# Optimization experiments

Hardware: AMD Instinct MI355X
Metric: run time of the kernel (lower is better)

Reference implementation:

```python
import jax, jax.numpy as jnp
import numpy as np

N = 2500   # total_neurons
K = 50     # connections_per_neuron
T = 60     # temporal_sequence
F = 5      # input_features
H = 128    # lstm hidden_size
B = 512    # batch
GROUPS = [800, 700, 600, 400]  # support_resistance, trend_detection, pattern_recognition, volume_analysis


def _lstm_layer(x, Wih, Whh, bih, bhh):
    # x: [B, T, D]; PyTorch gate order (i, f, g, o); eval mode (no dropout)
    bs = x.shape[0]
    h0 = jnp.zeros((bs, H), x.dtype)

    def step(carry, xt):
        h, c = carry
        g = xt @ Wih.T + h @ Whh.T + bih + bhh
        i, f, gg, o = jnp.split(g, 4, axis=-1)
        c = jax.nn.sigmoid(f) * c + jax.nn.sigmoid(i) * jnp.tanh(gg)
        h = jax.nn.sigmoid(o) * jnp.tanh(c)
        return (h, c), h

    (h, c), ys = jax.lax.scan(step, (h0, h0), jnp.swapaxes(x, 0, 1))
    return jnp.swapaxes(ys, 0, 1), h


def _forward(x, W_ih0, W_hh0, b_ih0, b_hh0, W_ih1, W_hh1, b_ih1, b_hh1,
             fp_w1, fp_b1, fp_w2, fp_b2, conn_w, sens, thr,
             int_w1, int_b1, int_w2, int_b2, int_w3, int_b3,
             tw, tb, pw, pb, kw, kb, vw, vb, cw, cb, conn_idx):
    y0, _ = _lstm_layer(x, W_ih0, W_hh0, b_ih0, b_hh0)
    _, hlast = _lstm_layer(y0, W_ih1, W_hh1, b_ih1, b_hh1)        # hidden[-1]: [B, H]
    base = jnp.tanh(jax.nn.relu(hlast @ fp_w1.T + fp_b1) @ fp_w2.T + fp_b2)  # [B, 32]
    # all_activations = base repeated over N neurons; each neuron reduces its
    # K gathered activations (weighted) and the identical 32 feature dims to a scalar.
    feat_sum = base.sum(-1)                                        # [B]
    acts = jnp.broadcast_to(feat_sum[:, None], (x.shape[0], N))    # [B, N]
    gathered = acts[:, conn_idx]                                   # [B, N, K] irregular gather
    wi = jnp.einsum('bnk,nk->bn', gathered, conn_w)                # [B, N]
    pre = wi * sens
    o0 = GROUPS[0]; o1 = o0 + GROUPS[1]; o2 = o1 + GROUPS[2]
    neuron_out = jnp.concatenate([
        jax.nn.sigmoid(pre[:, :o0] - thr[:o0]),                    # support_resistance
        jnp.tanh(pre[:, o0:o1]),                                   # trend_detection
        jax.nn.relu(pre[:, o1:o2] - thr[o1:o2]),                   # pattern_recognition
        jax.nn.sigmoid(pre[:, o2:]),                               # volume_analysis
    ], axis=1)                                                     # [B, N]
    h1 = jax.nn.relu(neuron_out @ int_w1.T + int_b1)
    h2 = jax.nn.relu(h1 @ int_w2.T + int_b2)
    integrated = jnp.tanh(h2 @ int_w3.T + int_b3)                  # [B, 32]
    trend = integrated @ tw.T + tb                                 # [B, 3]
    patt = integrated @ pw.T + pb                                  # [B, 6]
    keyl = integrated @ kw.T + kb                                  # [B, 4]
    vol = integrated @ vw.T + vb                                   # [B, 1]
    conf = integrated @ cw.T + cb                                  # [B, 1]
    means = jnp.stack([neuron_out[:, :o0].mean(1), neuron_out[:, o0:o1].mean(1),
                       neuron_out[:, o1:o2].mean(1), neuron_out[:, o2:].mean(1)], axis=-1)
    # heads(15) + raw confidence(1) + overall_confidence(1) + specialty means(4) -> [B, 21]? no: 3+6+4+1+1+1+4 = 20
    return jnp.concatenate([trend, patt, keyl, vol, conf, jax.nn.sigmoid(conf), means], axis=-1)


def setup_inputs() -> dict:
    key = jax.random.key(0)
    ks = jax.random.split(key, 40)
    rn = lambda k, s, sc=0.1: jax.random.normal(k, s, dtype=jnp.float32) * sc
    inp = {}
    inp['x'] = jax.random.normal(ks[0], (B, T, F), dtype=jnp.float32)
    inp['W_ih0'] = rn(ks[1], (4 * H, F)); inp['W_hh0'] = rn(ks[2], (4 * H, H))
    inp['b_ih0'] = rn(ks[3], (4 * H,));   inp['b_hh0'] = rn(ks[4], (4 * H,))
    inp['W_ih1'] = rn(ks[5], (4 * H, H)); inp['W_hh1'] = rn(ks[6], (4 * H, H))
    inp['b_ih1'] = rn(ks[7], (4 * H,));   inp['b_hh1'] = rn(ks[8], (4 * H,))
    inp['fp_w1'] = rn(ks[9], (64, H));    inp['fp_b1'] = rn(ks[10], (64,))
    inp['fp_w2'] = rn(ks[11], (32, 64));  inp['fp_b2'] = rn(ks[12], (32,))
    inp['conn_w'] = rn(ks[13], (N, K))
    inp['sens'] = 1.0 + rn(ks[14], (N,))
    inp['thr'] = 0.6 + rn(ks[15], (N,))
    inp['int_w1'] = rn(ks[16], (256, N), 0.02); inp['int_b1'] = rn(ks[17], (256,))
    inp['int_w2'] = rn(ks[18], (64, 256));      inp['int_b2'] = rn(ks[19], (64,))
    inp['int_w3'] = rn(ks[20], (32, 64));       inp['int_b3'] = rn(ks[21], (32,))
    inp['tw'] = rn(ks[22], (3, 32)); inp['tb'] = rn(ks[23], (3,))
    inp['pw'] = rn(ks[24], (6, 32)); inp['pb'] = rn(ks[25], (6,))
    inp['kw'] = rn(ks[26], (4, 32)); inp['kb'] = rn(ks[27], (4,))
    inp['vw'] = rn(ks[28], (1, 32)); inp['vb'] = rn(ks[29], (1,))
    inp['cw'] = rn(ks[30], (1, 32)); inp['cb'] = rn(ks[31], (1,))
    inp['conn_idx'] = jax.random.randint(ks[32], (N, K), 0, N)
    return inp


def reference(x, W_ih0, W_hh0, b_ih0, b_hh0, W_ih1, W_hh1, b_ih1, b_hh1,
              fp_w1, fp_b1, fp_w2, fp_b2, conn_w, sens, thr,
              int_w1, int_b1, int_w2, int_b2, int_w3, int_b3,
              tw, tb, pw, pb, kw, kb, vw, vb, cw, cb, conn_idx):
    return _forward(x, W_ih0, W_hh0, b_ih0, b_hh0, W_ih1, W_hh1, b_ih1, b_hh1,
                    fp_w1, fp_b1, fp_w2, fp_b2, conn_w, sens, thr,
                    int_w1, int_b1, int_w2, int_b2, int_w3, int_b3,
                    tw, tb, pw, pb, kw, kb, vw, vb, cw, cb, conn_idx)
```

## Files before the change

kernel.cpp:

```cpp
#include <hip/hip_runtime.h>
#include <math.h>

#define NB   512
#define TT   60
#define FF   5
#define HH   128
#define G4   512
#define NN   2500
#define KK   50

#define O0 800
#define O1 1500
#define O2 2100

#define OFF_B0F   0
#define OFF_B1F   40960
#define OFF_XA    106496
#define OFF_BIAS0 598016
#define OFF_BIAS1 598528
#define OFF_A     599040
#define OFF_FS    601540
#define OFF_H1    602052

#define PREP_T0 81920
#define PREP_T1 212992
#define PREP_T2 1196032
#define PREP_T3 1196544
#define PREP_T4 1197056
#define PREP_TOTAL 1199556

typedef _Float16 f16x8 __attribute__((ext_vector_type(8)));
typedef float f32x4 __attribute__((ext_vector_type(4)));

#define MFMA16(A, B, C) __builtin_amdgcn_mfma_f32_16x16x32_f16((A), (B), (C), 0, 0, 0)

__device__ __forceinline__ float sigf(float x) {
    return 1.0f / (1.0f + __expf(-x));
}
__device__ __forceinline__ float tanh2(float x) {
    float e = __expf(-2.0f * x);
    return fmaf(2.0f, 1.0f / (1.0f + e), -1.0f);
}

__global__ __launch_bounds__(256) void prep_kernel(
    const float* __restrict__ x,
    const float* __restrict__ W_ih0, const float* __restrict__ W_hh0,
    const float* __restrict__ b_ih0, const float* __restrict__ b_hh0,
    const float* __restrict__ W_ih1, const float* __restrict__ W_hh1,
    const float* __restrict__ b_ih1, const float* __restrict__ b_hh1,
    const float* __restrict__ conn_w, const float* __restrict__ sens,
    float* __restrict__ ws)
{
    int i = blockIdx.x * 256 + threadIdx.x;
    if (i >= PREP_TOTAL) return;

    if (i < PREP_T0) {
        int j = i & 7, l = (i >> 3) & 63;
        int rest = i >> 9;
        int g = rest & 3;
        int kbw = rest >> 2;
        int kb = kbw % 5, w = kbw / 5;
        int k = kb * 32 + (l >> 4) * 8 + j;
        int n = g * 128 + w * 16 + (l & 15);
        float val = 0.f;
        if (k < 128)       val = W_hh0[n * HH + k];
        else if (k < 133)  val = W_ih0[n * FF + (k - 128)];
        ((_Float16*)(ws + OFF_B0F))[i] = (_Float16)val;
    } else if (i < PREP_T1) {
        int v = i - PREP_T0;
        int j = v & 7, l = (v >> 3) & 63;
        int rest = v >> 9;
        int g = rest & 3;
        int kb = (rest >> 2) & 7;
        int w = rest >> 5;
        int k = kb * 32 + (l >> 4) * 8 + j;
        int n = g * 128 + w * 16 + (l & 15);
        float val = (k < 128) ? W_ih1[n * HH + k] : W_hh1[n * HH + (k - 128)];
        ((_Float16*)(ws + OFF_B1F))[v] = (_Float16)val;
    } else if (i < PREP_T2) {
        int v = i - PREP_T1;
        int j = v & 7, l = (v >> 3) & 63;
        int rest = v >> 9;
        int t = rest % 60, bb = rest / 60;
        float val = 0.f;
        if (l < 16 && j < 5)
            val = x[(bb * 16 + (l & 15)) * (TT * FF) + t * FF + j];
        ((_Float16*)(ws + OFF_XA))[v] = (_Float16)val;
    } else if (i < PREP_T3) {
        int j = i - PREP_T2;
        ws[OFF_BIAS0 + j] = b_ih0[j] + b_hh0[j];
    } else if (i < PREP_T4) {
        int j = i - PREP_T3;
        ws[OFF_BIAS1 + j] = b_ih1[j] + b_hh1[j];
    } else {
        int n = i - PREP_T4;
        float s = 0.f;
        const float* cw = conn_w + n * KK;
        for (int k = 0; k < KK; ++k) s += cw[k];
        ws[OFF_A + n] = s * sens[n];
    }
}

__global__ __launch_bounds__(512)
__attribute__((amdgpu_waves_per_eu(2, 2)))
void lstm_mfma(
    const float* __restrict__ ws_ro,
    const float* __restrict__ fp_w1, const float* __restrict__ fp_b1,
    const float* __restrict__ fp_w2, const float* __restrict__ fp_b2,
    float* __restrict__ feat_sum)
{
    __shared__ __align__(16) _Float16 hcat[2 * 4096];
    __shared__ float t1s[16][65];
    __shared__ float bss[16][33];

    const int tid = threadIdx.x;
    const int w = tid >> 6, l = tid & 63;
    const int u = w * 16 + (l & 15);
    const int row0 = (l >> 4) * 4;
    const int bb = blockIdx.x;

    ((uint4*)hcat)[tid] = make_uint4(0u, 0u, 0u, 0u);

    float bia0[4], bia1[4];
#pragma unroll
    for (int g = 0; g < 4; ++g) {
        bia0[g] = ws_ro[OFF_BIAS0 + g * 128 + u];
        bia1[g] = ws_ro[OFF_BIAS1 + g * 128 + u];
    }
    float c0[4] = {0.f, 0.f, 0.f, 0.f};
    float c1[4] = {0.f, 0.f, 0.f, 0.f};

    const f16x8* B0 = (const f16x8*)(ws_ro + OFF_B0F) + w * 20 * 64 + l;
    const f16x8* B1 = (const f16x8*)(ws_ro + OFF_B1F) + w * 32 * 64 + l;
    const f16x8* XA = (const f16x8*)(ws_ro + OFF_XA) + bb * 60 * 64 + l;
    const f16x8* HF = (const f16x8*)hcat;

    f16x8 wb1[32];
#pragma unroll
    for (int i = 0; i < 32; ++i) wb1[i] = B1[i * 64];

    const int h0base = (u >> 5) * 512 + ((u >> 3) & 3) * 128 + (u & 7);
    const int h1base = h0base + 2048;

    f16x8 xa = XA[0];

    __syncthreads();

    auto step = [&](int SRC, int DST, int t) {
        const f16x8* hs = HF + SRC * 512;
        const f16x8* hd = HF + DST * 512;
        _Float16* hw = hcat + DST * 4096;

        f16x8 xan = XA[(t + 1 < TT ? t + 1 : TT - 1) * 64];

        f32x4 a0 = {0.f,0.f,0.f,0.f}, a1 = {0.f,0.f,0.f,0.f};
        f32x4 a2 = {0.f,0.f,0.f,0.f}, a3 = {0.f,0.f,0.f,0.f};

        f16x8 s0 = B0[0*64],  s1 = B0[1*64],  s2 = B0[2*64],  s3 = B0[3*64];
        f16x8 r0 = B0[4*64],  r1 = B0[5*64],  r2 = B0[6*64],  r3 = B0[7*64];

        {
            f16x8 af = hs[0*64 + l];
            a0 = MFMA16(af, s0, a0); a1 = MFMA16(af, s1, a1);
            a2 = MFMA16(af, s2, a2); a3 = MFMA16(af, s3, a3);
        }
        s0 = B0[8*64];  s1 = B0[9*64];  s2 = B0[10*64]; s3 = B0[11*64];
        {
            f16x8 af = hs[1*64 + l];
            a0 = MFMA16(af, r0, a0); a1 = MFMA16(af, r1, a1);
            a2 = MFMA16(af, r2, a2); a3 = MFMA16(af, r3, a3);
        }
        r0 = B0[12*64]; r1 = B0[13*64]; r2 = B0[14*64]; r3 = B0[15*64];
        {
            f16x8 af = hs[2*64 + l];
            a0 = MFMA16(af, s0, a0); a1 = MFMA16(af, s1, a1);
            a2 = MFMA16(af, s2, a2); a3 = MFMA16(af, s3, a3);
        }
        s0 = B0[16*64]; s1 = B0[17*64]; s2 = B0[18*64]; s3 = B0[19*64];
        {
            f16x8 af = hs[3*64 + l];
            a0 = MFMA16(af, r0, a0); a1 = MFMA16(af, r1, a1);
            a2 = MFMA16(af, r2, a2); a3 = MFMA16(af, r3, a3);
        }
        {
            a0 = MFMA16(xa, s0, a0); a1 = MFMA16(xa, s1, a1);
            a2 = MFMA16(xa, s2, a2); a3 = MFMA16(xa, s3, a3);
        }

#pragma unroll
        for (int r = 0; r < 4; ++r) {
            float gi = sigf(a0[r] + bia0[0]);
            float gf = sigf(a1[r] + bia0[1]);
            float gg = tanh2(a2[r] + bia0[2]);
            float go = sigf(a3[r] + bia0[3]);
            c0[r] = gf * c0[r] + gi * gg;
            hw[h0base + (row0 + r) * 8] = (_Float16)(go * tanh2(c0[r]));
        }
        __syncthreads();

        f32x4 b0 = {0.f,0.f,0.f,0.f}, b1 = {0.f,0.f,0.f,0.f};
        f32x4 b2 = {0.f,0.f,0.f,0.f}, b3 = {0.f,0.f,0.f,0.f};
#pragma unroll
        for (int kb = 0; kb < 8; ++kb) {
            f16x8 af = (kb < 4) ? hd[kb * 64 + l] : hs[kb * 64 + l];
            b0 = MFMA16(af, wb1[kb*4+0], b0);
            b1 = MFMA16(af, wb1[kb*4+1], b1);
            b2 = MFMA16(af, wb1[kb*4+2], b2);
            b3 = MFMA16(af, wb1[kb*4+3], b3);
        }
#pragma unroll
        for (int r = 0; r < 4; ++r) {
            float gi = sigf(b0[r] + bia1[0]);
            float gf = sigf(b1[r] + bia1[1]);
            float gg = tanh2(b2[r] + bia1[2]);
            float go = sigf(b3[r] + bia1[3]);
            c1[r] = gf * c1[r] + gi * gg;
            hw[h1base + (row0 + r) * 8] = (_Float16)(go * tanh2(c1[r]));
        }
        __syncthreads();
        xa = xan;
    };

    for (int t = 0; t < TT; t += 2) {
        step(0, 1, t);
        step(1, 0, t + 1);
    }

    for (int idx = tid; idx < 16 * 64; idx += 512) {
        int r = idx >> 6, m = idx & 63;
        float acc = fp_b1[m];
        const float* wp = fp_w1 + m * HH;
        for (int k = 0; k < HH; ++k) {
            float hv = (float)hcat[2048 + (k >> 5) * 512 +
                                   (r + ((k >> 3) & 3) * 16) * 8 + (k & 7)];
            acc = fmaf(wp[k], hv, acc);
        }
        t1s[r][m] = fmaxf(acc, 0.f);
    }
    __syncthreads();
    if (tid < 16 * 32) {
        int r = tid >> 5, q = tid & 31;
        float acc = fp_b2[q];
        const float* wp = fp_w2 + q * 64;
        for (int m = 0; m < 64; ++m) acc = fmaf(wp[m], t1s[r][m], acc);
        bss[r][q] = tanh2(acc);
    }
    __syncthreads();
    if (tid < 16) {
        float s = 0.f;
        for (int q = 0; q < 32; ++q) s += bss[tid][q];
        feat_sum[bb * 16 + tid] = s;
    }
}

__device__ __forceinline__ float actn(int n, float pre, float th) {
    if (n < O0)       return sigf(pre - th);
    else if (n < O1)  return tanh2(pre);
    else if (n < O2)  return fmaxf(pre - th, 0.f);
    else              return sigf(pre);
}

__global__ __launch_bounds__(256) void gemm_h1(
    const float* __restrict__ feat_sum,
    const float* __restrict__ aw, const float* __restrict__ thr,
    const float* __restrict__ int_w1,
    const float* __restrict__ int_b1,
    float* __restrict__ h1)
{
    __shared__ float As[32][33];
    __shared__ float Bs[32][33];
    const int b0 = blockIdx.x * 32;
    const int m0 = blockIdx.y * 32;
    const int tid = threadIdx.x;
    const int ty = tid >> 4, tx = tid & 15;
    const int li = tid >> 3;
    const int lj = (tid & 7) * 4;

    const float s_li = feat_sum[b0 + li];

    float acc00 = 0.f, acc01 = 0.f, acc10 = 0.f, acc11 = 0.f;

    for (int k0 = 0; k0 < NN; k0 += 32) {
        float4 av = make_float4(0.f, 0.f, 0.f, 0.f);
        if (k0 + lj < NN) {
            float4 aa = *(const float4*)(aw + k0 + lj);
            float4 tt = *(const float4*)(thr + k0 + lj);
            int n = k0 + lj;
            av.x = actn(n + 0, s_li * aa.x, tt.x);
            av.y = actn(n + 1, s_li * aa.y, tt.y);
            av.z = actn(n + 2, s_li * aa.z, tt.z);
            av.w = actn(n + 3, s_li * aa.w, tt.w);
        }
        As[li][lj + 0] = av.x; As[li][lj + 1] = av.y;
        As[li][lj + 2] = av.z; As[li][lj + 3] = av.w;

        float4 wv = make_float4(0.f, 0.f, 0.f, 0.f);
        if (k0 + lj < NN)
            wv = *(const float4*)(int_w1 + (m0 + li) * NN + k0 + lj);
        Bs[lj + 0][li] = wv.x; Bs[lj + 1][li] = wv.y;
        Bs[lj + 2][li] = wv.z; Bs[lj + 3][li] = wv.w;
        __syncthreads();

#pragma unroll 8
        for (int kk = 0; kk < 32; ++kk) {
            float a0 = As[ty * 2][kk],  a1 = As[ty * 2 + 1][kk];
            float w0 = Bs[kk][tx * 2],  w1 = Bs[kk][tx * 2 + 1];
            acc00 += a0 * w0; acc01 += a0 * w1;
            acc10 += a1 * w0; acc11 += a1 * w1;
        }
        __syncthreads();
    }
    const int bi = b0 + ty * 2, mj = m0 + tx * 2;
    h1[bi * 256 + mj]           = fmaxf(acc00 + int_b1[mj], 0.f);
    h1[bi * 256 + mj + 1]       = fmaxf(acc01 + int_b1[mj + 1], 0.f);
    h1[(bi + 1) * 256 + mj]     = fmaxf(acc10 + int_b1[mj], 0.f);
    h1[(bi + 1) * 256 + mj + 1] = fmaxf(acc11 + int_b1[mj + 1], 0.f);
}

__global__ __launch_bounds__(64) void tail_kernel(
    const float* __restrict__ h1,
    const float* __restrict__ feat_sum,
    const float* __restrict__ aw, const float* __restrict__ thr,
    const float* __restrict__ int_w2, const float* __restrict__ int_b2,
    const float* __restrict__ int_w3, const float* __restrict__ int_b3,
    const float* __restrict__ tw, const float* __restrict__ tb,
    const float* __restrict__ pw, const float* __restrict__ pb,
    const float* __restrict__ kw, const float* __restrict__ kb,
    const float* __restrict__ vw, const float* __restrict__ vb,
    const float* __restrict__ cw, const float* __restrict__ cb,
    float* __restrict__ out)
{
    const int b = blockIdx.x;
    const int lane = threadIdx.x;
    __shared__ float h2s[64];
    __shared__ float ints[32];
    __shared__ float outs[16];
    __shared__ float red[4][64];
    __shared__ float mred[4];

    {
        const float s = feat_sum[b];
        float m0 = 0.f, m1 = 0.f, m2 = 0.f, m3 = 0.f;
        for (int n = lane; n < NN; n += 64) {
            float v = actn(n, s * aw[n], thr[n]);
            if (n < O0) m0 += v; else if (n < O1) m1 += v;
            else if (n < O2) m2 += v; else m3 += v;
        }
        red[0][lane] = m0; red[1][lane] = m1;
        red[2][lane] = m2; red[3][lane] = m3;
    }

    {
        float acc = int_b2[lane];
        const float* hp = h1 + b * 256;
        const float* wp = int_w2 + lane * 256;
        for (int m = 0; m < 256; ++m) acc += wp[m] * hp[m];
        h2s[lane] = fmaxf(acc, 0.f);
    }
    __syncthreads();
    if (lane < 4) {
        float acc = 0.f;
        for (int i = 0; i < 64; ++i) acc += red[lane][i];
        const float inv[4] = {1.f/800.f, 1.f/700.f, 1.f/600.f, 1.f/400.f};
        mred[lane] = acc * inv[lane];
    }
    if (lane < 32) {
        float acc = int_b3[lane];
        const float* wp = int_w3 + lane * 64;
        for (int m = 0; m < 64; ++m) acc += wp[m] * h2s[m];
        ints[lane] = tanh2(acc);
    }
    __syncthreads();
    if (lane < 15) {
        const float* wsel; float bsel;
        if (lane < 3)       { wsel = tw + lane * 32;       bsel = tb[lane]; }
        else if (lane < 9)  { wsel = pw + (lane - 3) * 32; bsel = pb[lane - 3]; }
        else if (lane < 13) { wsel = kw + (lane - 9) * 32; bsel = kb[lane - 9]; }
        else if (lane == 13){ wsel = vw;                   bsel = vb[0]; }
        else                { wsel = cw;                   bsel = cb[0]; }
        float acc = bsel;
        for (int q = 0; q < 32; ++q) acc += wsel[q] * ints[q];
        outs[lane] = acc;
    }
    __syncthreads();
    if (lane < 20) {
        float v;
        if (lane < 15)       v = outs[lane];
        else if (lane == 15) v = sigf(outs[14]);
        else                 v = mred[lane - 16];
        out[b * 20 + lane] = v;
    }
}

extern "C" void kernel_launch(void* const* d_in, const int* in_sizes, int n_in,
                              void* d_out, int out_size, void* d_ws, size_t ws_size,
                              hipStream_t stream)
{
    const float* x      = (const float*)d_in[0];
    const float* W_ih0  = (const float*)d_in[1];
    const float* W_hh0  = (const float*)d_in[2];
    const float* b_ih0  = (const float*)d_in[3];
    const float* b_hh0  = (const float*)d_in[4];
    const float* W_ih1  = (const float*)d_in[5];
    const float* W_hh1  = (const float*)d_in[6];
    const float* b_ih1  = (const float*)d_in[7];
    const float* b_hh1  = (const float*)d_in[8];
    const float* fp_w1  = (const float*)d_in[9];
    const float* fp_b1  = (const float*)d_in[10];
    const float* fp_w2  = (const float*)d_in[11];
    const float* fp_b2  = (const float*)d_in[12];
    const float* conn_w = (const float*)d_in[13];
    const float* sens   = (const float*)d_in[14];
    const float* thr    = (const float*)d_in[15];
    const float* int_w1 = (const float*)d_in[16];
    const float* int_b1 = (const float*)d_in[17];
    const float* int_w2 = (const float*)d_in[18];
    const float* int_b2 = (const float*)d_in[19];
    const float* int_w3 = (const float*)d_in[20];
    const float* int_b3 = (const float*)d_in[21];
    const float* tw     = (const float*)d_in[22];
    const float* tb     = (const float*)d_in[23];
    const float* pw     = (const float*)d_in[24];
    const float* pb     = (const float*)d_in[25];
    const float* kw     = (const float*)d_in[26];
    const float* kb     = (const float*)d_in[27];
    const float* vw     = (const float*)d_in[28];
    const float* vb     = (const float*)d_in[29];
    const float* cw     = (const float*)d_in[30];
    const float* cb     = (const float*)d_in[31];

    float* ws = (float*)d_ws;
    float* out = (float*)d_out;

    prep_kernel<<<(PREP_TOTAL + 255) / 256, 256, 0, stream>>>(
        x, W_ih0, W_hh0, b_ih0, b_hh0, W_ih1, W_hh1, b_ih1, b_hh1,
        conn_w, sens, ws);

    lstm_mfma<<<NB / 16, 512, 0, stream>>>(
        ws, fp_w1, fp_b1, fp_w2, fp_b2, ws + OFF_FS);

    {
        dim3 grid(NB / 32, 256 / 32);
        gemm_h1<<<grid, 256, 0, stream>>>(
            ws + OFF_FS, ws + OFF_A, thr, int_w1, int_b1, ws + OFF_H1);
    }

    tail_kernel<<<NB, 64, 0, stream>>>(
        ws + OFF_H1, ws + OFF_FS, ws + OFF_A, thr,
        int_w2, int_b2, int_w3, int_b3,
        tw, tb, pw, pb, kw, kb, vw, vb, cw, cb,
        out);
}
```

Measured before the change: 438.4 us.

## Stream layer-1 LSTM weights from cache instead of holding them in registers

Layer-1 recurrent weights are no longer kept as 32 register-resident f16x8 fragments. They are reloaded from global memory every step in a double-buffered s/r rotation, with the next step's layer-0 weights prefetched at the end of each step. The waves_per_eu(2,2) attribute is removed, and biases are folded into the accumulator initialisation. This lowers register pressure and the occupancy constraint, at the cost of more global or L2 weight traffic on the serial recurrence path, where load latency could stall the MFMAs.

```diff
diff --git a/kernel.cpp b/kernel.cpp
--- a/kernel.cpp
+++ b/kernel.cpp
@@ -101,9 +101,7 @@
     }
 }
 
-__global__ __launch_bounds__(512)
-__attribute__((amdgpu_waves_per_eu(2, 2)))
-void lstm_mfma(
+__global__ __launch_bounds__(512) void lstm_mfma(
     const float* __restrict__ ws_ro,
     const float* __restrict__ fp_w1, const float* __restrict__ fp_b1,
     const float* __restrict__ fp_w2, const float* __restrict__ fp_b2,
@@ -135,14 +133,13 @@
     const f16x8* XA = (const f16x8*)(ws_ro + OFF_XA) + bb * 60 * 64 + l;
     const f16x8* HF = (const f16x8*)hcat;
 
-    f16x8 wb1[32];
-#pragma unroll
-    for (int i = 0; i < 32; ++i) wb1[i] = B1[i * 64];
-
     const int h0base = (u >> 5) * 512 + ((u >> 3) & 3) * 128 + (u & 7);
     const int h1base = h0base + 2048;
 
     f16x8 xa = XA[0];
+
+    f16x8 s0 = B0[0*64], s1 = B0[1*64], s2 = B0[2*64], s3 = B0[3*64];
+    f16x8 r0 = B0[4*64], r1 = B0[5*64], r2 = B0[6*64], r3 = B0[7*64];
 
     __syncthreads();
 
@@ -153,11 +150,10 @@
 
         f16x8 xan = XA[(t + 1 < TT ? t + 1 : TT - 1) * 64];
 
-        f32x4 a0 = {0.f,0.f,0.f,0.f}, a1 = {0.f,0.f,0.f,0.f};
-        f32x4 a2 = {0.f,0.f,0.f,0.f}, a3 = {0.f,0.f,0.f,0.f};
-
-        f16x8 s0 = B0[0*64],  s1 = B0[1*64],  s2 = B0[2*64],  s3 = B0[3*64];
-        f16x8 r0 = B0[4*64],  r1 = B0[5*64],  r2 = B0[6*64],  r3 = B0[7*64];
+        f32x4 a0 = {bia0[0], bia0[0], bia0[0], bia0[0]};
+        f32x4 a1 = {bia0[1], bia0[1], bia0[1], bia0[1]};
+        f32x4 a2 = {bia0[2], bia0[2], bia0[2], bia0[2]};
+        f32x4 a3 = {bia0[3], bia0[3], bia0[3], bia0[3]};
 
         {
             f16x8 af = hs[0*64 + l];
@@ -182,38 +178,84 @@
             a0 = MFMA16(af, r0, a0); a1 = MFMA16(af, r1, a1);
             a2 = MFMA16(af, r2, a2); a3 = MFMA16(af, r3, a3);
         }
+        r0 = B1[0*64];  r1 = B1[1*64];  r2 = B1[2*64];  r3 = B1[3*64];
         {
             a0 = MFMA16(xa, s0, a0); a1 = MFMA16(xa, s1, a1);
             a2 = MFMA16(xa, s2, a2); a3 = MFMA16(xa, s3, a3);
         }
+        s0 = B1[4*64];  s1 = B1[5*64];  s2 = B1[6*64];  s3 = B1[7*64];
 
 #pragma unroll
         for (int r = 0; r < 4; ++r) {
-            float gi = sigf(a0[r] + bia0[0]);
-            float gf = sigf(a1[r] + bia0[1]);
-            float gg = tanh2(a2[r] + bia0[2]);
-            float go = sigf(a3[r] + bia0[3]);
+            float gi = sigf(a0[r]);
+            float gf = sigf(a1[r]);
+            float gg = tanh2(a2[r]);
+            float go = sigf(a3[r]);
             c0[r] = gf * c0[r] + gi * gg;
             hw[h0base + (row0 + r) * 8] = (_Float16)(go * tanh2(c0[r]));
         }
         __syncthreads();
 
-        f32x4 b0 = {0.f,0.f,0.f,0.f}, b1 = {0.f,0.f,0.f,0.f};
-        f32x4 b2 = {0.f,0.f,0.f,0.f}, b3 = {0.f,0.f,0.f,0.f};
-#pragma unroll
-        for (int kb = 0; kb < 8; ++kb) {
-            f16x8 af = (kb < 4) ? hd[kb * 64 + l] : hs[kb * 64 + l];
-            b0 = MFMA16(af, wb1[kb*4+0], b0);
-            b1 = MFMA16(af, wb1[kb*4+1], b1);
-            b2 = MFMA16(af, wb1[kb*4+2], b2);
-            b3 = MFMA16(af, wb1[kb*4+3], b3);
-        }
+        f32x4 b0 = {bia1[0], bia1[0], bia1[0], bia1[0]};
+        f32x4 b1 = {bia1[1], bia1[1], bia1[1], bia1[1]};
+        f32x4 b2 = {bia1[2], bia1[2], bia1[2], bia1[2]};
+        f32x4 b3 = {bia1[3], bia1[3], bia1[3], bia1[3]};
+
+        {
+            f16x8 af = hd[0*64 + l];
+            b0 = MFMA16(af, r0, b0); b1 = MFMA16(af, r1, b1);
+            b2 = MFMA16(af, r2, b2); b3 = MFMA16(af, r3, b3);
+        }
+        r0 = B1[8*64];  r1 = B1[9*64];  r2 = B1[10*64]; r3 = B1[11*64];
+        {
+            f16x8 af = hd[1*64 + l];
+            b0 = MFMA16(af, s0, b0); b1 = MFMA16(af, s1, b1);
+            b2 = MFMA16(af, s2, b2); b3 = MFMA16(af, s3, b3);
+        }
+        s0 = B1[12*64]; s1 = B1[13*64]; s2 = B1[14*64]; s3 = B1[15*64];
+        {
+            f16x8 af = hd[2*64 + l];
+            b0 = MFMA16(af, r0, b0); b1 = MFMA16(af, r1, b1);
+            b2 = MFMA16(af, r2, b2); b3 = MFMA16(af, r3, b3);
+        }
+        r0 = B1[16*64]; r1 = B1[17*64]; r2 = B1[18*64]; r3 = B1[19*64];
+        {
+            f16x8 af = hd[3*64 + l];
+            b0 = MFMA16(af, s0, b0); b1 = MFMA16(af, s1, b1);
+            b2 = MFMA16(af, s2, b2); b3 = MFMA16(af, s3, b3);
+        }
+        s0 = B1[20*64]; s1 = B1[21*64]; s2 = B1[22*64]; s3 = B1[23*64];
+        {
+            f16x8 af = hs[4*64 + l];
+            b0 = MFMA16(af, r0, b0); b1 = MFMA16(af, r1, b1);
+            b2 = MFMA16(af, r2, b2); b3 = MFMA16(af, r3, b3);
+        }
+        r0 = B1[24*64]; r1 = B1[25*64]; r2 = B1[26*64]; r3 = B1[27*64];
+        {
+            f16x8 af = hs[5*64 + l];
+            b0 = MFMA16(af, s0, b0); b1 = MFMA16(af, s1, b1);
+            b2 = MFMA16(af, s2, b2); b3 = MFMA16(af, s3, b3);
+        }
+        s0 = B1[28*64]; s1 = B1[29*64]; s2 = B1[30*64]; s3 = B1[31*64];
+        {
+            f16x8 af = hs[6*64 + l];
+            b0 = MFMA16(af, r0, b0); b1 = MFMA16(af, r1, b1);
+            b2 = MFMA16(af, r2, b2); b3 = MFMA16(af, r3, b3);
+        }
+        r0 = B0[4*64];  r1 = B0[5*64];  r2 = B0[6*64];  r3 = B0[7*64];
+        {
+            f16x8 af = hs[7*64 + l];
+            b0 = MFMA16(af, s0, b0); b1 = MFMA16(af, s1, b1);
+            b2 = MFMA16(af, s2, b2); b3 = MFMA16(af, s3, b3);
+        }
+        s0 = B0[0*64];  s1 = B0[1*64];  s2 = B0[2*64];  s3 = B0[3*64];
+
 #pragma unroll
         for (int r = 0; r < 4; ++r) {
-            float gi = sigf(b0[r] + bia1[0]);
-            float gf = sigf(b1[r] + bia1[1]);
-            float gg = tanh2(b2[r] + bia1[2]);
-            float go = sigf(b3[r] + bia1[3]);
+            float gi = sigf(b0[r]);
+            float gf = sigf(b1[r]);
+            float gg = tanh2(b2[r]);
+            float go = sigf(b3[r]);
             c1[r] = gf * c1[r] + gi * gg;
             hw[h1base + (row0 + r) * 8] = (_Float16)(go * tanh2(c1[r]));
         }
```

Measured after the change: 489.4 us. 11.6% more time.
